# Kernel optimization log

Measured on AMD Instinct MI355X. Metric: run time of the kernel, lower is better.

The kernel has to match this reference:

```python
import jax, jax.numpy as jnp
import numpy as np

EPS_BN = 1e-5


def conv_bn_relu(x, w, b, gamma, beta):
    # x: (B, Cin, N); w: (Cout, Cin) -> pointwise Conv1d (kernel=1)
    y = jnp.einsum('oc,bcn->bon', w, x) + b[None, :, None]
    # BatchNorm1d in training mode: stats over (batch, length) per channel
    mean = y.mean(axis=(0, 2), keepdims=True)
    var = y.var(axis=(0, 2), keepdims=True)
    y = (y - mean) * jax.lax.rsqrt(var + EPS_BN)
    y = gamma[None, :, None] * y + beta[None, :, None]
    return jax.nn.relu(y)


def wls_jet_fit_order1(points, weights):
    # points: (B, 3, N) neighborhood coords; weights: (B, N)
    B, _, N = points.shape
    px, py, pz = points[:, 0], points[:, 1], points[:, 2]  # each (B, N)
    # if too few weights are significant, fall back to uniform weights
    valid = jnp.sum(weights > 1e-3, axis=1, keepdims=True) > 18  # (B, 1)
    w = jnp.where(valid, weights, jnp.ones_like(weights))        # (B, N)
    # order-1 jet: plane z = b0*x + b1*y + b2
    A = jnp.stack([px, py, jnp.ones_like(px)], axis=2)           # (B, N, 3)
    XtX = jnp.einsum('bnd,bn,bne->bde', A, w, A)                 # (B, 3, 3)
    XtY = jnp.einsum('bnd,bn,bn->bd', A, w, pz)                  # (B, 3)
    beta = jnp.linalg.solve(XtX, XtY[..., None])[..., 0]         # (B, 3)
    n = jnp.concatenate([-beta[:, 0:2], jnp.ones((B, 1), beta.dtype)], axis=1)
    n = n / jnp.linalg.norm(n, axis=1, keepdims=True)            # unit normal
    return beta, n


def setup_inputs() -> dict:
    key = jax.random.key(0)
    ks = jax.random.split(key, 8)
    B, C, N = 512, 1024, 256
    inp = {
        'points': jax.random.normal(ks[0], (B, 3, N), dtype=jnp.float32),
        'x': jax.random.normal(ks[1], (B, C, N), dtype=jnp.float32),
        'n_effective_points': jax.random.randint(ks[2], (B,), 0, N),
        # conv weights (Cout, Cin) and biases
        'w1': jax.random.normal(ks[3], (512, 1024), dtype=jnp.float32) * 0.02,
        'b1': jnp.zeros((512,), jnp.float32),
        'g1': jnp.ones((512,), jnp.float32),
        'be1': jnp.zeros((512,), jnp.float32),
        'w2': jax.random.normal(ks[4], (256, 512), dtype=jnp.float32) * 0.02,
        'b2': jnp.zeros((256,), jnp.float32),
        'g2': jnp.ones((256,), jnp.float32),
        'be2': jnp.zeros((256,), jnp.float32),
        'w3': jax.random.normal(ks[5], (128, 256), dtype=jnp.float32) * 0.02,
        'b3': jnp.zeros((128,), jnp.float32),
        'g3': jnp.ones((128,), jnp.float32),
        'be3': jnp.zeros((128,), jnp.float32),
        'w4': jax.random.normal(ks[6], (1, 128), dtype=jnp.float32) * 0.02,
        'b4': jnp.zeros((1,), jnp.float32),
    }
    return inp


def reference(points, x, n_effective_points,
              w1, b1, g1, be1, w2, b2, g2, be2, w3, b3, g3, be3, w4, b4):
    h = conv_bn_relu(x, w1, b1, g1, be1)   # (B, 512, N)
    h = conv_bn_relu(h, w2, b2, g2, be2)   # (B, 256, N)
    h = conv_bn_relu(h, w3, b3, g3, be3)   # (B, 128, N)
    logits = jnp.einsum('oc,bcn->bon', w4, h) + b4[None, :, None]  # (B, 1, N)
    weights = 0.01 + jax.nn.sigmoid(logits)[:, 0]                  # (B, N)
    beta, normal = wls_jet_fit_order1(points, weights)
    # neighbor_normals and residuals are None for this config; omitted
    return (normal, beta, weights)
```

## Files before the change

### kernel.cpp

```cpp
#include <hip/hip_runtime.h>
#include <hip/hip_bf16.h>

typedef __attribute__((ext_vector_type(8))) short short8;
typedef __attribute__((ext_vector_type(4))) float f32x4;

typedef __attribute__((address_space(1))) const void GV;
typedef __attribute__((address_space(3))) void LV;

__device__ __forceinline__ unsigned short f2bf(float f) {
  union { float f; unsigned u; } v; v.f = f;
  unsigned r = v.u + 0x7fffu + ((v.u >> 16) & 1u);
  return (unsigned short)(r >> 16);
}
__device__ __forceinline__ float bf2f(unsigned short s) {
  union { unsigned u; float f; } v; v.u = ((unsigned)s) << 16;
  return v.f;
}

__global__ __launch_bounds__(256) void convert_weights(
    const float* __restrict__ w1, const float* __restrict__ w2, const float* __restrict__ w3,
    unsigned short* __restrict__ w1b, unsigned short* __restrict__ w2b, unsigned short* __restrict__ w3b) {
  int i = blockIdx.x * 256 + threadIdx.x;
  if (i < 524288) w1b[i] = f2bf(w1[i]);
  if (i < 131072) w2b[i] = f2bf(w2[i]);
  if (i < 32768)  w3b[i] = f2bf(w3[i]);
}

__global__ __launch_bounds__(256) void transpose_x(const float* __restrict__ x,
                                                   unsigned short* __restrict__ xT) {
  __shared__ float tile[64][65];
  int bid = blockIdx.x;
  int nt = bid & 3, ct = (bid >> 2) & 15, b = bid >> 6;
  int c0 = ct << 6, n0 = nt << 6;
  int tx = threadIdx.x & 63, ty = threadIdx.x >> 6;
  const float* xp = x + ((size_t)b * 1024 + c0) * 256 + n0;
  #pragma unroll
  for (int r = ty; r < 64; r += 4) tile[r][tx] = xp[(size_t)r * 256 + tx];
  __syncthreads();
  unsigned short* op = xT + ((size_t)b * 256 + n0) * 1024 + c0;
  int cc = (threadIdx.x & 31) * 2;
  #pragma unroll
  for (int rn = threadIdx.x >> 5; rn < 64; rn += 8) {
    ushort2 o2; o2.x = f2bf(tile[cc][rn]); o2.y = f2bf(tile[cc + 1][rn]);
    *reinterpret_cast<ushort2*>(op + (size_t)rn * 1024 + cc) = o2;
  }
}

template<int M, int K>
__global__ __launch_bounds__(256, 2) void gemm_bn(
    const unsigned short* __restrict__ W, const unsigned short* __restrict__ X,
    unsigned short* __restrict__ Y, float* __restrict__ stat) {
  constexpr int NMT = M / 128;
  __shared__ unsigned short As[128 * 32];
  __shared__ unsigned short Bs[128 * 32];
  __shared__ float bsum[128], bsq[128];

  int tid = threadIdx.x, bid = blockIdx.x;
  int nt = bid & 1;
  int mt = (bid >> 1) % NMT;
  int b  = bid / (2 * NMT);
  int wid = tid >> 6, lane = tid & 63;
  int wr = wid >> 1, wc = wid & 1;
  int m0 = mt * 128, n0 = nt * 128;

  if (tid < 128) { bsum[tid] = 0.f; bsq[tid] = 0.f; }

  const unsigned short* Ag = W + (size_t)m0 * K;
  const unsigned short* Bg = X + ((size_t)b * 256 + n0) * K;

  int cA = wid * 64 + lane;
  int rowA = cA >> 2, colA = (cA & 3) * 8;

  f32x4 acc[4][4];
  #pragma unroll
  for (int i = 0; i < 4; ++i)
    #pragma unroll
    for (int j = 0; j < 4; ++j)
      #pragma unroll
      for (int r = 0; r < 4; ++r) acc[i][j][r] = 0.f;

  char* AsW = (char*)As + wid * 1024;
  char* BsW = (char*)Bs + wid * 1024;
  int lrow = lane & 15, lk = (lane >> 4) * 16;

  for (int kt = 0; kt < K / 32; ++kt) {
    int k0 = kt * 32;
    __syncthreads();
    __builtin_amdgcn_global_load_lds((GV*)(Ag + (size_t)rowA * K + k0 + colA), (LV*)AsW, 16, 0, 0);
    __builtin_amdgcn_global_load_lds((GV*)(Ag + (size_t)(rowA + 64) * K + k0 + colA), (LV*)(AsW + 4096), 16, 0, 0);
    __builtin_amdgcn_global_load_lds((GV*)(Bg + (size_t)rowA * K + k0 + colA), (LV*)BsW, 16, 0, 0);
    __builtin_amdgcn_global_load_lds((GV*)(Bg + (size_t)(rowA + 64) * K + k0 + colA), (LV*)(BsW + 4096), 16, 0, 0);
    __syncthreads();
    short8 af[4], bfv[4];
    #pragma unroll
    for (int i = 0; i < 4; ++i) {
      af[i]  = *reinterpret_cast<const short8*>((const char*)As + (wr * 64 + i * 16 + lrow) * 64 + lk);
      bfv[i] = *reinterpret_cast<const short8*>((const char*)Bs + (wc * 64 + i * 16 + lrow) * 64 + lk);
    }
    #pragma unroll
    for (int i = 0; i < 4; ++i)
      #pragma unroll
      for (int j = 0; j < 4; ++j)
        acc[i][j] = __builtin_amdgcn_mfma_f32_16x16x32_bf16(af[i], bfv[j], acc[i][j], 0, 0, 0);
  }

  size_t ybase = (size_t)b * 256 * M;
  int group = lane >> 4;
  #pragma unroll
  for (int mi = 0; mi < 4; ++mi) {
    int o0 = m0 + wr * 64 + mi * 16 + group * 4;
    #pragma unroll
    for (int ni = 0; ni < 4; ++ni) {
      int n = n0 + wc * 64 + ni * 16 + lrow;
      ushort4 pk;
      pk.x = f2bf(acc[mi][ni][0]);
      pk.y = f2bf(acc[mi][ni][1]);
      pk.z = f2bf(acc[mi][ni][2]);
      pk.w = f2bf(acc[mi][ni][3]);
      *reinterpret_cast<ushort4*>(Y + ybase + (size_t)n * M + o0) = pk;
    }
  }
  #pragma unroll
  for (int mi = 0; mi < 4; ++mi) {
    #pragma unroll
    for (int r = 0; r < 4; ++r) {
      float s = 0.f, q = 0.f;
      #pragma unroll
      for (int ni = 0; ni < 4; ++ni) { float v = acc[mi][ni][r]; s += v; q += v * v; }
      #pragma unroll
      for (int msk = 1; msk < 16; msk <<= 1) {
        s += __shfl_xor(s, msk, 64);
        q += __shfl_xor(q, msk, 64);
      }
      if (lrow == 0) {
        int ol = wr * 64 + mi * 16 + group * 4 + r;
        atomicAdd(&bsum[ol], s);
        atomicAdd(&bsq[ol], q);
      }
    }
  }
  __syncthreads();
  if (tid < 128) {
    atomicAdd(&stat[(m0 + tid) * 2],     bsum[tid]);
    atomicAdd(&stat[(m0 + tid) * 2 + 1], bsq[tid]);
  }
}

template<int M>
__global__ void finalize_stats(const float* __restrict__ stat, const float* __restrict__ g,
                               const float* __restrict__ be, float* __restrict__ aArr,
                               float* __restrict__ cArr) {
  int i = blockIdx.x * 64 + threadIdx.x;
  if (i >= M) return;
  const float inv = 1.0f / 131072.0f;
  float mean = stat[2 * i] * inv;
  float var  = stat[2 * i + 1] * inv - mean * mean;
  float rstd = rsqrtf(var + 1e-5f);
  float a = g[i] * rstd;
  aArr[i] = a;
  cArr[i] = be[i] - a * mean;
}

template<int M>
__global__ __launch_bounds__(256) void bn_relu(unsigned short* __restrict__ Y,
                                               const float* __restrict__ aArr,
                                               const float* __restrict__ cArr) {
  int idx = blockIdx.x * 256 + threadIdx.x;
  int o0 = (idx % (M / 8)) * 8;
  uint4 u = *reinterpret_cast<const uint4*>(Y + (size_t)idx * 8);
  float4 a0 = *reinterpret_cast<const float4*>(aArr + o0);
  float4 a1 = *reinterpret_cast<const float4*>(aArr + o0 + 4);
  float4 c0 = *reinterpret_cast<const float4*>(cArr + o0);
  float4 c1 = *reinterpret_cast<const float4*>(cArr + o0 + 4);
  const unsigned short* pu = reinterpret_cast<const unsigned short*>(&u);
  float va[8] = {a0.x, a0.y, a0.z, a0.w, a1.x, a1.y, a1.z, a1.w};
  float vc[8] = {c0.x, c0.y, c0.z, c0.w, c1.x, c1.y, c1.z, c1.w};
  uint4 outv;
  unsigned short* po = reinterpret_cast<unsigned short*>(&outv);
  #pragma unroll
  for (int j = 0; j < 8; ++j) {
    float h = fmaxf(va[j] * bf2f(pu[j]) + vc[j], 0.f);
    po[j] = f2bf(h);
  }
  *reinterpret_cast<uint4*>(Y + (size_t)idx * 8) = outv;
}

__global__ __launch_bounds__(256) void final_fit(
    const unsigned short* __restrict__ H,
    const float* __restrict__ w4, const float* __restrict__ b4,
    const float* __restrict__ points,
    float* __restrict__ out) {
  int b = blockIdx.x, n = threadIdx.x;
  __shared__ float w4s[128];
  __shared__ float red[4][9];
  if (n < 128) w4s[n] = w4[n];
  __syncthreads();

  const unsigned short* h = H + ((size_t)b * 256 + n) * 128;
  float logit = b4[0];
  #pragma unroll
  for (int i = 0; i < 16; ++i) {
    uint4 u = *reinterpret_cast<const uint4*>(h + i * 8);
    const unsigned short* pu = reinterpret_cast<const unsigned short*>(&u);
    #pragma unroll
    for (int j = 0; j < 8; ++j) logit += w4s[i * 8 + j] * bf2f(pu[j]);
  }
  float wgt = 0.01f + 1.0f / (1.0f + expf(-logit));
  out[3072 + b * 256 + n] = wgt;

  const float* p = points + (size_t)b * 768;
  float px = p[n], py = p[256 + n], pz = p[512 + n];
  float v[9] = {wgt * px * px, wgt * px * py, wgt * px, wgt * py * py, wgt * py,
                wgt, wgt * px * pz, wgt * py * pz, wgt * pz};
  #pragma unroll
  for (int k = 0; k < 9; ++k)
    #pragma unroll
    for (int msk = 1; msk < 64; msk <<= 1) v[k] += __shfl_xor(v[k], msk, 64);
  int wid = n >> 6, lane = n & 63;
  if (lane == 0)
    #pragma unroll
    for (int k = 0; k < 9; ++k) red[wid][k] = v[k];
  __syncthreads();
  if (n == 0) {
    double S[9];
    #pragma unroll
    for (int k = 0; k < 9; ++k)
      S[k] = (double)red[0][k] + red[1][k] + red[2][k] + red[3][k];
    double a11 = S[0], a12 = S[1], a13 = S[2], a22 = S[3], a23 = S[4], a33 = S[5];
    double t1 = S[6], t2 = S[7], t3 = S[8];
    double d  = a11 * (a22 * a33 - a23 * a23) - a12 * (a12 * a33 - a23 * a13) + a13 * (a12 * a23 - a22 * a13);
    double b0 = (t1 * (a22 * a33 - a23 * a23) - a12 * (t2 * a33 - a23 * t3) + a13 * (t2 * a23 - a22 * t3)) / d;
    double b1 = (a11 * (t2 * a33 - t3 * a23) - t1 * (a12 * a33 - a23 * a13) + a13 * (a12 * t3 - t2 * a13)) / d;
    double b2 = (a11 * (a22 * t3 - a23 * t2) - a12 * (a12 * t3 - t2 * a13) + t1 * (a12 * a23 - a13 * a22)) / d;
    double nn = sqrt(b0 * b0 + b1 * b1 + 1.0);
    out[b * 3 + 0] = (float)(-b0 / nn);
    out[b * 3 + 1] = (float)(-b1 / nn);
    out[b * 3 + 2] = (float)(1.0 / nn);
    out[1536 + b * 3 + 0] = (float)b0;
    out[1536 + b * 3 + 1] = (float)b1;
    out[1536 + b * 3 + 2] = (float)b2;
  }
}

extern "C" void kernel_launch(void* const* d_in, const int* in_sizes, int n_in,
                              void* d_out, int out_size, void* d_ws, size_t ws_size,
                              hipStream_t stream) {
  const float* points = (const float*)d_in[0];
  const float* x   = (const float*)d_in[1];
  const float* w1  = (const float*)d_in[3];
  const float* g1  = (const float*)d_in[5];
  const float* be1 = (const float*)d_in[6];
  const float* w2  = (const float*)d_in[7];
  const float* g2  = (const float*)d_in[9];
  const float* be2 = (const float*)d_in[10];
  const float* w3  = (const float*)d_in[11];
  const float* g3  = (const float*)d_in[13];
  const float* be3 = (const float*)d_in[14];
  const float* w4  = (const float*)d_in[15];
  const float* b4  = (const float*)d_in[16];
  float* out = (float*)d_out;

  char* ws = (char*)d_ws;
  unsigned short* xT  = (unsigned short*)(ws);
  unsigned short* y2  = (unsigned short*)(ws);
  unsigned short* y3  = (unsigned short*)(ws + 67108864);
  unsigned short* y1  = (unsigned short*)(ws + 268435456);
  unsigned short* w1b = (unsigned short*)(ws + 402653184);
  unsigned short* w2b = (unsigned short*)(ws + 403701760);
  unsigned short* w3b = (unsigned short*)(ws + 403963904);
  float* stat1 = (float*)(ws + 404029440);
  float* stat2 = stat1 + 1024;
  float* stat3 = stat2 + 512;
  float* a1 = stat3 + 256; float* c1 = a1 + 512;
  float* a2 = c1 + 512;    float* c2 = a2 + 256;
  float* a3 = c2 + 256;    float* c3 = a3 + 128;

  hipMemsetAsync(stat1, 0, (1024 + 512 + 256) * sizeof(float), stream);
  convert_weights<<<2048, 256, 0, stream>>>(w1, w2, w3, w1b, w2b, w3b);
  transpose_x<<<32768, 256, 0, stream>>>(x, xT);

  gemm_bn<512, 1024><<<4096, 256, 0, stream>>>(w1b, xT, y1, stat1);
  finalize_stats<512><<<8, 64, 0, stream>>>(stat1, g1, be1, a1, c1);
  bn_relu<512><<<32768, 256, 0, stream>>>(y1, a1, c1);

  gemm_bn<256, 512><<<2048, 256, 0, stream>>>(w2b, y1, y2, stat2);
  finalize_stats<256><<<4, 64, 0, stream>>>(stat2, g2, be2, a2, c2);
  bn_relu<256><<<16384, 256, 0, stream>>>(y2, a2, c2);

  gemm_bn<128, 256><<<1024, 256, 0, stream>>>(w3b, y2, y3, stat3);
  finalize_stats<128><<<2, 64, 0, stream>>>(stat3, g3, be3, a3, c3);
  bn_relu<128><<<8192, 256, 0, stream>>>(y3, a3, c3);

  final_fit<<<512, 256, 0, stream>>>(y3, w4, b4, points, out);
}
```

Measured before the change: 1.229 ms.

## Fuse BN+ReLU into next GEMM's operand load and drop bn_relu kernels

Removes the standalone bn_relu passes. The per-channel scale, shift and ReLU are now applied as the next GEMM loads its B operand, and in final_fit for the last layer. The fused GEMM loads B through registers instead of the direct global-to-LDS path, so each element is transformed as it is written to LDS. Block indices are also remapped across 8 groups, likely for XCD locality, and the occupancy hint in launch_bounds is dropped. This saves one read and one write of each intermediate activation, at the cost of extra ALU work and register pressure inside the GEMM load stage.

```diff
diff --git a/kernel.cpp b/kernel.cpp
--- a/kernel.cpp
+++ b/kernel.cpp
@@ -46,27 +46,30 @@
   }
 }
 
-template<int M, int K>
-__global__ __launch_bounds__(256, 2) void gemm_bn(
+template<int M, int K, bool FUSE>
+__global__ __launch_bounds__(256) void gemm_bn(
     const unsigned short* __restrict__ W, const unsigned short* __restrict__ X,
+    const float* __restrict__ aIn, const float* __restrict__ cIn,
     unsigned short* __restrict__ Y, float* __restrict__ stat) {
   constexpr int NMT = M / 128;
+  constexpr int NWG = (131072 / 128) * NMT;
   __shared__ unsigned short As[128 * 32];
   __shared__ unsigned short Bs[128 * 32];
   __shared__ float bsum[128], bsq[128];
 
-  int tid = threadIdx.x, bid = blockIdx.x;
-  int nt = bid & 1;
-  int mt = (bid >> 1) % NMT;
-  int b  = bid / (2 * NMT);
+  int tid = threadIdx.x;
+  int orig = blockIdx.x;
+  int wg = (orig & 7) * (NWG / 8) + (orig >> 3);
+  int mt = wg % NMT;
+  int rt = wg / NMT;
   int wid = tid >> 6, lane = tid & 63;
   int wr = wid >> 1, wc = wid & 1;
-  int m0 = mt * 128, n0 = nt * 128;
+  int m0 = mt * 128;
 
   if (tid < 128) { bsum[tid] = 0.f; bsq[tid] = 0.f; }
 
   const unsigned short* Ag = W + (size_t)m0 * K;
-  const unsigned short* Bg = X + ((size_t)b * 256 + n0) * K;
+  const unsigned short* Bg = X + (size_t)rt * 128 * K;
 
   int cA = wid * 64 + lane;
   int rowA = cA >> 2, colA = (cA & 3) * 8;
@@ -82,14 +85,50 @@
   char* AsW = (char*)As + wid * 1024;
   char* BsW = (char*)Bs + wid * 1024;
   int lrow = lane & 15, lk = (lane >> 4) * 16;
+
+  const unsigned short* bsrc0 = Bg + (size_t)rowA * K + colA;
+  const unsigned short* bsrc1 = bsrc0 + (size_t)64 * K;
+  char* bdst0 = (char*)Bs + rowA * 64 + (cA & 3) * 16;
+  char* bdst1 = bdst0 + 4096;
 
   for (int kt = 0; kt < K / 32; ++kt) {
     int k0 = kt * 32;
     __syncthreads();
     __builtin_amdgcn_global_load_lds((GV*)(Ag + (size_t)rowA * K + k0 + colA), (LV*)AsW, 16, 0, 0);
     __builtin_amdgcn_global_load_lds((GV*)(Ag + (size_t)(rowA + 64) * K + k0 + colA), (LV*)(AsW + 4096), 16, 0, 0);
-    __builtin_amdgcn_global_load_lds((GV*)(Bg + (size_t)rowA * K + k0 + colA), (LV*)BsW, 16, 0, 0);
-    __builtin_amdgcn_global_load_lds((GV*)(Bg + (size_t)(rowA + 64) * K + k0 + colA), (LV*)(BsW + 4096), 16, 0, 0);
+    if constexpr (!FUSE) {
+      __builtin_amdgcn_global_load_lds((GV*)(Bg + (size_t)rowA * K + k0 + colA), (LV*)BsW, 16, 0, 0);
+      __builtin_amdgcn_global_load_lds((GV*)(Bg + (size_t)(rowA + 64) * K + k0 + colA), (LV*)(BsW + 4096), 16, 0, 0);
+    } else {
+      uint4 u0 = *reinterpret_cast<const uint4*>(bsrc0 + k0);
+      uint4 u1 = *reinterpret_cast<const uint4*>(bsrc1 + k0);
+      int ch0 = k0 + colA;
+      float4 alo = *reinterpret_cast<const float4*>(aIn + ch0);
+      float4 ahi = *reinterpret_cast<const float4*>(aIn + ch0 + 4);
+      float4 clo = *reinterpret_cast<const float4*>(cIn + ch0);
+      float4 chi = *reinterpret_cast<const float4*>(cIn + ch0 + 4);
+      float va[8] = {alo.x, alo.y, alo.z, alo.w, ahi.x, ahi.y, ahi.z, ahi.w};
+      float vc[8] = {clo.x, clo.y, clo.z, clo.w, chi.x, chi.y, chi.z, chi.w};
+      ushort4 p0, p1;
+      const unsigned short* s0 = reinterpret_cast<const unsigned short*>(&u0);
+      const unsigned short* s1 = reinterpret_cast<const unsigned short*>(&u1);
+      unsigned short* o0 = reinterpret_cast<unsigned short*>(&p0);
+      unsigned short* o1 = reinterpret_cast<unsigned short*>(&p1);
+      ushort4 q0, q1;
+      unsigned short* o0b = reinterpret_cast<unsigned short*>(&q0);
+      unsigned short* o1b = reinterpret_cast<unsigned short*>(&q1);
+      #pragma unroll
+      for (int j = 0; j < 4; ++j) {
+        o0[j]  = f2bf(fmaxf(va[j]     * bf2f(s0[j])     + vc[j],     0.f));
+        o0b[j] = f2bf(fmaxf(va[j + 4] * bf2f(s0[j + 4]) + vc[j + 4], 0.f));
+        o1[j]  = f2bf(fmaxf(va[j]     * bf2f(s1[j])     + vc[j],     0.f));
+        o1b[j] = f2bf(fmaxf(va[j + 4] * bf2f(s1[j + 4]) + vc[j + 4], 0.f));
+      }
+      *reinterpret_cast<ushort4*>(bdst0)     = p0;
+      *reinterpret_cast<ushort4*>(bdst0 + 8) = q0;
+      *reinterpret_cast<ushort4*>(bdst1)     = p1;
+      *reinterpret_cast<ushort4*>(bdst1 + 8) = q1;
+    }
     __syncthreads();
     short8 af[4], bfv[4];
     #pragma unroll
@@ -104,20 +143,19 @@
         acc[i][j] = __builtin_amdgcn_mfma_f32_16x16x32_bf16(af[i], bfv[j], acc[i][j], 0, 0, 0);
   }
 
-  size_t ybase = (size_t)b * 256 * M;
   int group = lane >> 4;
   #pragma unroll
   for (int mi = 0; mi < 4; ++mi) {
     int o0 = m0 + wr * 64 + mi * 16 + group * 4;
     #pragma unroll
     for (int ni = 0; ni < 4; ++ni) {
-      int n = n0 + wc * 64 + ni * 16 + lrow;
+      int row = rt * 128 + wc * 64 + ni * 16 + lrow;
       ushort4 pk;
       pk.x = f2bf(acc[mi][ni][0]);
       pk.y = f2bf(acc[mi][ni][1]);
       pk.z = f2bf(acc[mi][ni][2]);
       pk.w = f2bf(acc[mi][ni][3]);
-      *reinterpret_cast<ushort4*>(Y + ybase + (size_t)n * M + o0) = pk;
+      *reinterpret_cast<ushort4*>(Y + (size_t)row * M + o0) = pk;
     }
   }
   #pragma unroll
@@ -161,39 +199,16 @@
   cArr[i] = be[i] - a * mean;
 }
 
-template<int M>
-__global__ __launch_bounds__(256) void bn_relu(unsigned short* __restrict__ Y,
-                                               const float* __restrict__ aArr,
-                                               const float* __restrict__ cArr) {
-  int idx = blockIdx.x * 256 + threadIdx.x;
-  int o0 = (idx % (M / 8)) * 8;
-  uint4 u = *reinterpret_cast<const uint4*>(Y + (size_t)idx * 8);
-  float4 a0 = *reinterpret_cast<const float4*>(aArr + o0);
-  float4 a1 = *reinterpret_cast<const float4*>(aArr + o0 + 4);
-  float4 c0 = *reinterpret_cast<const float4*>(cArr + o0);
-  float4 c1 = *reinterpret_cast<const float4*>(cArr + o0 + 4);
-  const unsigned short* pu = reinterpret_cast<const unsigned short*>(&u);
-  float va[8] = {a0.x, a0.y, a0.z, a0.w, a1.x, a1.y, a1.z, a1.w};
-  float vc[8] = {c0.x, c0.y, c0.z, c0.w, c1.x, c1.y, c1.z, c1.w};
-  uint4 outv;
-  unsigned short* po = reinterpret_cast<unsigned short*>(&outv);
-  #pragma unroll
-  for (int j = 0; j < 8; ++j) {
-    float h = fmaxf(va[j] * bf2f(pu[j]) + vc[j], 0.f);
-    po[j] = f2bf(h);
-  }
-  *reinterpret_cast<uint4*>(Y + (size_t)idx * 8) = outv;
-}
-
 __global__ __launch_bounds__(256) void final_fit(
     const unsigned short* __restrict__ H,
+    const float* __restrict__ a3, const float* __restrict__ c3,
     const float* __restrict__ w4, const float* __restrict__ b4,
     const float* __restrict__ points,
     float* __restrict__ out) {
   int b = blockIdx.x, n = threadIdx.x;
-  __shared__ float w4s[128];
+  __shared__ float w4s[128], as3[128], cs3[128];
   __shared__ float red[4][9];
-  if (n < 128) w4s[n] = w4[n];
+  if (n < 128) { w4s[n] = w4[n]; as3[n] = a3[n]; cs3[n] = c3[n]; }
   __syncthreads();
 
   const unsigned short* h = H + ((size_t)b * 256 + n) * 128;
@@ -203,7 +218,11 @@
     uint4 u = *reinterpret_cast<const uint4*>(h + i * 8);
     const unsigned short* pu = reinterpret_cast<const unsigned short*>(&u);
     #pragma unroll
-    for (int j = 0; j < 8; ++j) logit += w4s[i * 8 + j] * bf2f(pu[j]);
+    for (int j = 0; j < 8; ++j) {
+      int ch = i * 8 + j;
+      float hv = fmaxf(as3[ch] * bf2f(pu[j]) + cs3[ch], 0.f);
+      logit += w4s[ch] * hv;
+    }
   }
   float wgt = 0.01f + 1.0f / (1.0f + expf(-logit));
   out[3072 + b * 256 + n] = wgt;
@@ -279,17 +298,14 @@
   convert_weights<<<2048, 256, 0, stream>>>(w1, w2, w3, w1b, w2b, w3b);
   transpose_x<<<32768, 256, 0, stream>>>(x, xT);
 
-  gemm_bn<512, 1024><<<4096, 256, 0, stream>>>(w1b, xT, y1, stat1);
+  gemm_bn<512, 1024, false><<<4096, 256, 0, stream>>>(w1b, xT, nullptr, nullptr, y1, stat1);
   finalize_stats<512><<<8, 64, 0, stream>>>(stat1, g1, be1, a1, c1);
-  bn_relu<512><<<32768, 256, 0, stream>>>(y1, a1, c1);
-
-  gemm_bn<256, 512><<<2048, 256, 0, stream>>>(w2b, y1, y2, stat2);
+
+  gemm_bn<256, 512, true><<<2048, 256, 0, stream>>>(w2b, y1, a1, c1, y2, stat2);
   finalize_stats<256><<<4, 64, 0, stream>>>(stat2, g2, be2, a2, c2);
-  bn_relu<256><<<16384, 256, 0, stream>>>(y2, a2, c2);
-
-  gemm_bn<128, 256><<<1024, 256, 0, stream>>>(w3b, y2, y3, stat3);
+
+  gemm_bn<128, 256, true><<<1024, 256, 0, stream>>>(w3b, y2, a2, c2, y3, stat3);
   finalize_stats<128><<<2, 64, 0, stream>>>(stat3, g3, be3, a3, c3);
-  bn_relu<128><<<8192, 256, 0, stream>>>(y3, a3, c3);
-
-  final_fit<<<512, 256, 0, stream>>>(y3, w4, b4, points, out);
-}
+
+  final_fit<<<512, 256, 0, stream>>>(y3, a3, c3, w4, b4, points, out);
+}
```

Result: no change. 1.237 ms (+0.7%).
